# Kernel tuning notes

Measured on AMD Instinct MI355X. Metric: run time of the kernel, lower is better.

Reference implementation:

```python
import jax, jax.numpy as jnp
import numpy as np
jax.config.update("jax_enable_x64", True)  # subchunk uses float64 decays (T=128 > 24)

B, T, D = 4, 2048, 1024
H, K = 16, 64            # head_size = 64, D = H*K
CHUNK = 128              # T % 128 == 0 -> only the 128-chunk path of _chunked_wkv runs
DMIX, DDEC = 32, 64      # D_MIX_DIM, D_DECAY_DIM
PREC_MIN = 0.005
LN_EPS = 1e-5 * 8.0 ** 2 # eps * head_size_divisor**2


def setup_inputs() -> dict:
    key = jax.random.key(0)
    ks = jax.random.split(key, 24)
    f32 = jnp.float32
    rn = lambda k, s, sc=1.0: (jax.random.normal(k, s) * sc).astype(f32)
    un = lambda k, s, lo, hi: jax.random.uniform(k, s, minval=lo, maxval=hi).astype(f32)
    inv_sq = 1.0 / np.sqrt(D)
    return {
        "x": rn(ks[0], (B, T, D)),
        # token-mix interpolation coefficients (init-like: in [0,1])
        "time_maa_x": un(ks[1], (1, 1, D), 0.0, 1.0),
        "time_maa_w": un(ks[2], (1, 1, D), 0.0, 1.0),
        "time_maa_k": un(ks[3], (1, 1, D), 0.0, 1.0),
        "time_maa_v": un(ks[4], (1, 1, D), 0.0, 1.0),
        "time_maa_r": un(ks[5], (1, 1, D), 0.0, 1.0),
        "time_maa_g": un(ks[6], (1, 1, D), 0.0, 1.0),
        "time_maa_w1": rn(ks[7], (D, 5 * DMIX), 0.01),
        "time_maa_w2": un(ks[8], (5, DMIX, D), -0.01, 0.01),
        # decay: init range roughly [-6, -1] like the module
        "time_decay": un(ks[9], (1, 1, D), -6.0, -1.0),
        "time_decay_w1": rn(ks[10], (D, DDEC), 0.01),
        "time_decay_w2": un(ks[11], (DDEC, D), -0.01, 0.01),
        "time_faaaa": un(ks[12], (H, K), -0.1, 0.5),
        # projections (stored [in, out]; x @ W == nn.Linear)
        "Wr": rn(ks[13], (D, D), inv_sq),
        "Wk": rn(ks[14], (D, D), inv_sq),
        "Wv": rn(ks[15], (D, D), inv_sq),
        "Wg": rn(ks[16], (D, D), inv_sq),
        "Wo": rn(ks[17], (D, D), inv_sq),
        "ln_w": jnp.ones((D,), f32),
        "ln_b": jnp.zeros((D,), f32),
    }


def _causal_shift(x):
    # x[t-1], zero at t=0
    return jnp.pad(x[:, :-1, :], ((0, 0), (1, 0), (0, 0)))


def _chunked_wkv(r, k, v, w, u, state):
    # r,k,v,w: [B,H,L,K]; u: [1,H,1,K]; state: [B,H,K,V]
    Bb, Hh, L, Kk = r.shape
    V = v.shape[-1]
    Tc = CHUNK
    N = L // Tc
    f64 = jnp.float64

    w_decay = jnp.clip(jnp.exp(w), PREC_MIN, None)
    wc_log = jnp.log(w_decay.astype(jnp.float32)).reshape(Bb, Hh, N, Tc, Kk)
    wc_cum = jnp.cumsum(wc_log, axis=-2)                              # inclusive cumsum over chunk
    shifted = jnp.pad(wc_cum[..., :-1, :], ((0, 0),) * 3 + ((1, 0), (0, 0)))
    ws = wc_log.sum(axis=-2, keepdims=True)                           # [B,H,N,1,K] total log-decay
    w_inter = jnp.exp(ws - wc_cum).astype(r.dtype)
    w_intra = jnp.exp(wc_cum - wc_log).astype(r.dtype)

    rc = r.reshape(Bb, Hh, N, Tc, Kk)
    kc = k.reshape(Bb, Hh, N, Tc, Kk)
    vc = v.reshape(Bb, Hh, N, Tc, V)

    # intra-chunk attention in float64 with mid-chunk offset for stability
    off = shifted[..., Tc // 2:Tc // 2 + 1, :]
    r_decay = jnp.exp((shifted - off).astype(f64))
    k_inv = jnp.exp((off - wc_cum).astype(f64))
    a = jnp.einsum('bhnik,bhnjk->bhnij', rc.astype(f64) * r_decay,
                   kc.astype(f64) * k_inv).astype(r.dtype)
    a = jnp.tril(a, -1)
    diag = jnp.einsum('bhntk,bhntk->bhnt', rc, u[:, :, :, None, :] * kc)  # u bonus on the diagonal
    a = a + diag[..., None] * jnp.eye(Tc, dtype=r.dtype)
    out = jnp.einsum('bhnij,bhnjv->bhniv', a, vc)

    # inter-chunk recurrent state carry
    wkv = jnp.einsum('bhntk,bhntv->bhnkv', kc * w_inter, vc)          # per-chunk KV update
    ws_e = jnp.swapaxes(jnp.exp(ws), -1, -2).astype(r.dtype)          # [B,H,N,K,1]

    def step(s, xs):
        wkv_i, ws_i = xs
        return s * ws_i + wkv_i, s                                    # emit state BEFORE update

    state_f, states = jax.lax.scan(step, state,
                                   (jnp.moveaxis(wkv, 2, 0), jnp.moveaxis(ws_e, 2, 0)))
    states = jnp.moveaxis(states, 0, 2)                               # [B,H,N,K,V]
    out = out + jnp.einsum('bhntk,bhnkv->bhntv', rc * w_intra, states)
    return out.reshape(Bb, Hh, L, V), state_f


def reference(x, time_maa_x, time_maa_w, time_maa_k, time_maa_v, time_maa_r,
              time_maa_g, time_maa_w1, time_maa_w2, time_decay, time_decay_w1,
              time_decay_w2, time_faaaa, Wr, Wk, Wv, Wg, Wo, ln_w, ln_b):
    Bb, Tt, Dd = x.shape
    xx = _causal_shift(x) - x                                          # dxprev (recurrent mode)

    # data-dependent 5-way token-mix (RWKV-6 LoRA mix)
    xxx = jnp.tanh((x + xx * time_maa_x) @ time_maa_w1)                # [B,T,5*DMIX]
    m = jnp.einsum('btfi,fid->fbtd', xxx.reshape(Bb, Tt, 5, DMIX), time_maa_w2)
    mw, mk, mv, mr, mg = m
    xw = x + xx * (time_maa_w + mw)
    xk = x + xx * (time_maa_k + mk)
    xv = x + xx * (time_maa_v + mv)
    xr = x + xx * (time_maa_r + mr)
    xg = x + xx * (time_maa_g + mg)

    to_heads = lambda t: t.reshape(Bb, Tt, H, K).transpose(0, 2, 1, 3)  # [B,H,T,K]
    r = to_heads(xr @ Wr)
    k = to_heads(xk @ Wk)
    v = to_heads(xv @ Wv)
    g = jax.nn.silu(xg @ Wg)

    ww = time_decay + jnp.tanh(xw @ time_decay_w1) @ time_decay_w2
    w = to_heads(-jnp.exp(ww))                                         # log-decay (negative)
    u = time_faaaa.reshape(1, H, 1, K)

    state0 = jnp.zeros((Bb, H, K, K), dtype=x.dtype)
    out, _state = _chunked_wkv(r, k, v, w, u, state0)

    # GroupNorm(n_head groups) over flattened (B*T, D)
    og = out.transpose(0, 2, 1, 3).reshape(Bb * Tt, H, K)
    mu = og.mean(-1, keepdims=True)
    var = og.var(-1, keepdims=True)
    og = (og - mu) / jnp.sqrt(var + LN_EPS)
    out = (og.reshape(Bb * Tt, Dd) * ln_w + ln_b).reshape(Bb, Tt, Dd)

    return (out * g) @ Wo
```

## Files before the change

### kernel.cpp

```cpp
#include <hip/hip_runtime.h>
#include <hip/hip_bf16.h>
#include <math.h>

typedef __hip_bfloat16 bf16;
typedef __attribute__((ext_vector_type(8))) short short8;
typedef __attribute__((ext_vector_type(4))) float f32x4;

#define Tt 2048
#define Dd 1024
#define Hh 16

__device__ __forceinline__ float b2f(bf16 v){ return __bfloat162float(v); }
__device__ __forceinline__ bf16  f2b(float v){ return __float2bfloat16(v); }

__device__ __forceinline__ int seg_t(int lr, int t0, int Lm1){ return t0 + (lr & Lm1); }
__device__ __forceinline__ size_t seg_grow(int lr, int b0, int t0, int Llog2, int Lm1){
  return ((size_t)(b0 + (lr >> Llog2)) * Tt) + (size_t)seg_t(lr, t0, Lm1);
}

struct MixP { const bf16* maa[5]; bf16* dst[5]; };
struct Proj4 { const bf16* A[4]; const bf16* Bt[4]; bf16* C[4]; };

__global__ __launch_bounds__(256) void k_detect(const unsigned short* __restrict__ xs,
                                                int* __restrict__ flag){
  __shared__ int bad;
  if(threadIdx.x == 0) bad = 0;
  __syncthreads();
  int local = 0;
  for(int i = threadIdx.x; i < 8192; i += 256){
    unsigned e = (xs[i] >> 7) & 0xFF;
    if(e >= 0xC0) local++;
  }
  if(local) atomicAdd(&bad, local);
  __syncthreads();
  if(threadIdx.x == 0) flag[0] = (bad > 16) ? 1 : 0;
}

__global__ __launch_bounds__(256) void k_conv(const void* __restrict__ src,
                                              bf16* __restrict__ dst, int n,
                                              const int* __restrict__ flag){
  int i = blockIdx.x * 256 + threadIdx.x;
  if(i >= n) return;
  if(flag[0]) dst[i] = f2b(((const float*)src)[i]);
  else        dst[i] = ((const bf16*)src)[i];
}

__global__ __launch_bounds__(256) void k_transpose(const bf16* __restrict__ src,
                                                   bf16* __restrict__ dst){
  __shared__ bf16 tile[32][33];
  int bx = blockIdx.x * 32, by = blockIdx.y * 32;
  int tx = threadIdx.x & 31, ty = threadIdx.x >> 5;
  for(int r = ty; r < 32; r += 8)
    tile[r][tx] = src[(size_t)(by + r) * 1024 + bx + tx];
  __syncthreads();
  for(int r = ty; r < 32; r += 8)
    dst[(size_t)(bx + r) * 1024 + by + tx] = tile[tx][r];
}

__global__ __launch_bounds__(256) void k_transposeP(const bf16* __restrict__ src,
                                                    bf16* __restrict__ dst,
                                                    int K, int N, int Npad){
  int idx = blockIdx.x * 256 + threadIdx.x;
  if(idx >= Npad * K) return;
  int n = idx / K, k = idx - n * K;
  dst[idx] = (n < N) ? src[(size_t)k * N + n] : f2b(0.f);
}

__global__ __launch_bounds__(256) void k_prep(const bf16* __restrict__ x,
                                              const bf16* __restrict__ tmx,
                                              bf16* __restrict__ xmx,
                                              int b0, int t0, int Llog2){
  const int Lm1 = (1 << Llog2) - 1;
  int idx = blockIdx.x * 256 + threadIdx.x;
  int lr = idx >> 10, d = idx & 1023;
  size_t grow = seg_grow(lr, b0, t0, Llog2, Lm1);
  int tl = seg_t(lr, t0, Lm1);
  float xc = b2f(x[grow * Dd + d]);
  float xp = tl ? b2f(x[(grow - 1) * Dd + d]) : 0.f;
  xmx[idx] = f2b(xc + (xp - xc) * b2f(tmx[d]));
}

constexpr int GEPI_BF16 = 0, GEPI_SILU = 1, GEPI_OUT = 2;

template<int EPI>
__global__ __launch_bounds__(256) void gemm_mfma(
    const bf16* __restrict__ A,
    const bf16* __restrict__ Bt,
    void* __restrict__ Cv,
    const int* __restrict__ oflag,
    int rowoff){
  __shared__ short As[128 * 40];
  __shared__ short Bs[128 * 40];
  int tid = threadIdx.x;
  int bn = blockIdx.x * 128;
  int bm = blockIdx.y * 128;
  int w = tid >> 6, lane = tid & 63;
  int wm = (w & 1) * 64, wn = (w >> 1) * 64;
  int m16 = lane & 15, quad = lane >> 4;

  f32x4 acc[4][4];
  #pragma unroll
  for(int mi = 0; mi < 4; mi++)
    #pragma unroll
    for(int ni = 0; ni < 4; ni++)
      acc[mi][ni] = (f32x4){0.f, 0.f, 0.f, 0.f};

  int srow = tid >> 2;
  int sk8  = (tid & 3) * 8;
  const bf16* Ag = A  + (size_t)(bm + srow) * 1024 + sk8;
  const bf16* Bg = Bt + (size_t)(bn + srow) * 1024 + sk8;
  short* Aw = As + srow * 40 + sk8;
  short* Bw = Bs + srow * 40 + sk8;

  for(int kb = 0; kb < 1024; kb += 32){
    #pragma unroll
    for(int rep = 0; rep < 2; rep++){
      *(short8*)(Aw + rep * 64 * 40) = *(const short8*)(Ag + (size_t)rep * 64 * 1024 + kb);
      *(short8*)(Bw + rep * 64 * 40) = *(const short8*)(Bg + (size_t)rep * 64 * 1024 + kb);
    }
    __syncthreads();
    short8 af[4], bfr[4];
    #pragma unroll
    for(int mi = 0; mi < 4; mi++)
      af[mi] = *(const short8*)(As + (wm + mi * 16 + m16) * 40 + quad * 8);
    #pragma unroll
    for(int ni = 0; ni < 4; ni++)
      bfr[ni] = *(const short8*)(Bs + (wn + ni * 16 + m16) * 40 + quad * 8);
    #pragma unroll
    for(int mi = 0; mi < 4; mi++)
      #pragma unroll
      for(int ni = 0; ni < 4; ni++)
        acc[mi][ni] = __builtin_amdgcn_mfma_f32_16x16x32_bf16(af[mi], bfr[ni], acc[mi][ni], 0, 0, 0);
    __syncthreads();
  }
  #pragma unroll
  for(int mi = 0; mi < 4; mi++){
    #pragma unroll
    for(int ni = 0; ni < 4; ni++){
      #pragma unroll
      for(int r = 0; r < 4; r++){
        int row = bm + wm + mi * 16 + quad * 4 + r;
        int col = bn + wn + ni * 16 + m16;
        float v = acc[mi][ni][r];
        if constexpr(EPI == GEPI_BF16){
          ((bf16*)Cv)[(size_t)row * 1024 + col] = f2b(v);
        } else if constexpr(EPI == GEPI_SILU){
          ((bf16*)Cv)[(size_t)row * 1024 + col] = f2b(v / (1.f + expf(-v)));
        } else {
          size_t off = (size_t)(row + rowoff) * 1024 + col;
          if(oflag[0]) ((float*)Cv)[off] = v;
          else         ((bf16*)Cv)[off]  = f2b(v);
        }
      }
    }
  }
}

__global__ __launch_bounds__(256) void gemm_proj4(Proj4 prm){
  int z = blockIdx.z;
  const bf16* __restrict__ A  = prm.A[z];
  const bf16* __restrict__ Bt = prm.Bt[z];
  bf16* __restrict__ C        = prm.C[z];
  __shared__ short As[128 * 40];
  __shared__ short Bs[128 * 40];
  int tid = threadIdx.x;
  int bn = blockIdx.x * 128;
  int bm = blockIdx.y * 128;
  int w = tid >> 6, lane = tid & 63;
  int wm = (w & 1) * 64, wn = (w >> 1) * 64;
  int m16 = lane & 15, quad = lane >> 4;

  f32x4 acc[4][4];
  #pragma unroll
  for(int mi = 0; mi < 4; mi++)
    #pragma unroll
    for(int ni = 0; ni < 4; ni++)
      acc[mi][ni] = (f32x4){0.f, 0.f, 0.f, 0.f};

  int srow = tid >> 2;
  int sk8  = (tid & 3) * 8;
  const bf16* Ag = A  + (size_t)(bm + srow) * 1024 + sk8;
  const bf16* Bg = Bt + (size_t)(bn + srow) * 1024 + sk8;
  short* Aw = As + srow * 40 + sk8;
  short* Bw = Bs + srow * 40 + sk8;

  for(int kb = 0; kb < 1024; kb += 32){
    #pragma unroll
    for(int rep = 0; rep < 2; rep++){
      *(short8*)(Aw + rep * 64 * 40) = *(const short8*)(Ag + (size_t)rep * 64 * 1024 + kb);
      *(short8*)(Bw + rep * 64 * 40) = *(const short8*)(Bg + (size_t)rep * 64 * 1024 + kb);
    }
    __syncthreads();
    short8 af[4], bfr[4];
    #pragma unroll
    for(int mi = 0; mi < 4; mi++)
      af[mi] = *(const short8*)(As + (wm + mi * 16 + m16) * 40 + quad * 8);
    #pragma unroll
    for(int ni = 0; ni < 4; ni++)
      bfr[ni] = *(const short8*)(Bs + (wn + ni * 16 + m16) * 40 + quad * 8);
    #pragma unroll
    for(int mi = 0; mi < 4; mi++)
      #pragma unroll
      for(int ni = 0; ni < 4; ni++)
        acc[mi][ni] = __builtin_amdgcn_mfma_f32_16x16x32_bf16(af[mi], bfr[ni], acc[mi][ni], 0, 0, 0);
    __syncthreads();
  }
  bool silu = (z == 3);
  #pragma unroll
  for(int mi = 0; mi < 4; mi++){
    #pragma unroll
    for(int ni = 0; ni < 4; ni++){
      #pragma unroll
      for(int r = 0; r < 4; r++){
        int row = bm + wm + mi * 16 + quad * 4 + r;
        int col = bn + wn + ni * 16 + m16;
        float v = acc[mi][ni][r];
        if(silu) v = v / (1.f + expf(-v));
        C[(size_t)row * 1024 + col] = f2b(v);
      }
    }
  }
}

__global__ __launch_bounds__(256) void gemm_mix(
    const bf16* __restrict__ xxx,
    const bf16* __restrict__ w2T,
    const bf16* __restrict__ xg,
    MixP prm, int b0, int t0, int Llog2){
  const int Lm1 = (1 << Llog2) - 1;
  int c = blockIdx.z;
  __shared__ short As[128 * 40];
  __shared__ short Bs[128 * 40];
  int tid = threadIdx.x;
  int bn = blockIdx.x * 128;
  int bm = blockIdx.y * 128;
  int w = tid >> 6, lane = tid & 63;
  int wm = (w & 1) * 64, wn = (w >> 1) * 64;
  int m16 = lane & 15, quad = lane >> 4;

  int srow = tid >> 2;
  int sk8  = (tid & 3) * 8;
  #pragma unroll
  for(int rep = 0; rep < 2; rep++){
    *(short8*)(As + (srow + rep * 64) * 40 + sk8) =
        *(const short8*)(xxx + (size_t)(bm + srow + rep * 64) * 256 + c * 32 + sk8);
    *(short8*)(Bs + (srow + rep * 64) * 40 + sk8) =
        *(const short8*)(w2T + (size_t)c * 32768 + (size_t)(bn + srow + rep * 64) * 32 + sk8);
  }
  __syncthreads();
  f32x4 acc[4][4];
  short8 af[4], bfr[4];
  #pragma unroll
  for(int mi = 0; mi < 4; mi++)
    af[mi] = *(const short8*)(As + (wm + mi * 16 + m16) * 40 + quad * 8);
  #pragma unroll
  for(int ni = 0; ni < 4; ni++)
    bfr[ni] = *(const short8*)(Bs + (wn + ni * 16 + m16) * 40 + quad * 8);
  #pragma unroll
  for(int mi = 0; mi < 4; mi++)
    #pragma unroll
    for(int ni = 0; ni < 4; ni++)
      acc[mi][ni] = __builtin_amdgcn_mfma_f32_16x16x32_bf16(
          af[mi], bfr[ni], (f32x4){0.f, 0.f, 0.f, 0.f}, 0, 0, 0);

  const bf16* maa = prm.maa[c];
  bf16* dst = prm.dst[c];
  #pragma unroll
  for(int mi = 0; mi < 4; mi++){
    #pragma unroll
    for(int ni = 0; ni < 4; ni++){
      #pragma unroll
      for(int r = 0; r < 4; r++){
        int row = bm + wm + mi * 16 + quad * 4 + r;
        int col = bn + wn + ni * 16 + m16;
        size_t grow = seg_grow(row, b0, t0, Llog2, Lm1);
        int tl = seg_t(row, t0, Lm1);
        float xc = b2f(xg[grow * Dd + col]);
        float xp = tl ? b2f(xg[(grow - 1) * Dd + col]) : 0.f;
        dst[(size_t)row * 1024 + col] =
            f2b(xc + (xp - xc) * (b2f(maa[col]) + acc[mi][ni][r]));
      }
    }
  }
}

constexpr int G2_TANH = 0, G2_DECAY = 1;

template<int EPI>
__global__ __launch_bounds__(256) void gemm_mfma2(
    const bf16* __restrict__ A,
    const bf16* __restrict__ Bt,
    void* __restrict__ Cv, int ldc,
    int Ndim, int Kdim,
    const bf16* __restrict__ e_w){
  __shared__ short As[128 * 40];
  __shared__ short Bs[128 * 40];
  int tid = threadIdx.x;
  int bn = blockIdx.x * 128;
  int bm = blockIdx.y * 128;
  int w = tid >> 6, lane = tid & 63;
  int wm = (w & 1) * 64, wn = (w >> 1) * 64;
  int m16 = lane & 15, quad = lane >> 4;

  f32x4 acc[4][4];
  #pragma unroll
  for(int mi = 0; mi < 4; mi++)
    #pragma unroll
    for(int ni = 0; ni < 4; ni++)
      acc[mi][ni] = (f32x4){0.f, 0.f, 0.f, 0.f};

  int srow = tid >> 2;
  int sk8  = (tid & 3) * 8;
  const bf16* Ag = A  + (size_t)(bm + srow) * Kdim + sk8;
  const bf16* Bg = Bt + (size_t)(bn + srow) * Kdim + sk8;
  short* Aw = As + srow * 40 + sk8;
  short* Bw = Bs + srow * 40 + sk8;

  for(int kb = 0; kb < Kdim; kb += 32){
    #pragma unroll
    for(int rep = 0; rep < 2; rep++){
      *(short8*)(Aw + rep * 64 * 40) = *(const short8*)(Ag + (size_t)rep * 64 * Kdim + kb);
      *(short8*)(Bw + rep * 64 * 40) = *(const short8*)(Bg + (size_t)rep * 64 * Kdim + kb);
    }
    __syncthreads();
    short8 af[4], bfr[4];
    #pragma unroll
    for(int mi = 0; mi < 4; mi++)
      af[mi] = *(const short8*)(As + (wm + mi * 16 + m16) * 40 + quad * 8);
    #pragma unroll
    for(int ni = 0; ni < 4; ni++)
      bfr[ni] = *(const short8*)(Bs + (wn + ni * 16 + m16) * 40 + quad * 8);
    #pragma unroll
    for(int mi = 0; mi < 4; mi++)
      #pragma unroll
      for(int ni = 0; ni < 4; ni++)
        acc[mi][ni] = __builtin_amdgcn_mfma_f32_16x16x32_bf16(af[mi], bfr[ni], acc[mi][ni], 0, 0, 0);
    __syncthreads();
  }
  #pragma unroll
  for(int mi = 0; mi < 4; mi++){
    #pragma unroll
    for(int ni = 0; ni < 4; ni++){
      #pragma unroll
      for(int r = 0; r < 4; r++){
        int row = bm + wm + mi * 16 + quad * 4 + r;
        int col = bn + wn + ni * 16 + m16;
        if(col >= Ndim) continue;
        float v = acc[mi][ni][r];
        size_t off = (size_t)row * ldc + col;
        if constexpr(EPI == G2_TANH){
          ((bf16*)Cv)[off] = f2b(tanhf(v));
        } else {
          float td = b2f(e_w[col]) + v;
          ((float*)Cv)[off] = fmaxf(-expf(td), -5.2983173665480363f);
        }
      }
    }
  }
}

constexpr int EPI_OUTV = 5;
#define BM 64
#define BN 64
#define BK 16

template<int EPI>
__global__ __launch_bounds__(256) void gemm_ep(
    const bf16* __restrict__ A, int lda,
    const bf16* __restrict__ Bm, int ldb,
    void* __restrict__ Cv, int ldc,
    int Mdim, int Ndim, int Kdim,
    const bf16* __restrict__ xg, const bf16* __restrict__ e_w,
    int b0, int t0, int Llog2, const int* __restrict__ oflag){
  const int Lm1 = (1 << Llog2) - 1;
  __shared__ float As[BM][BK + 1];
  __shared__ float Bs[BK][BN + 4];
  int tid = threadIdx.x;
  int tx = tid & 15, ty = tid >> 4;
  int bm = blockIdx.y * BM, bn = blockIdx.x * BN;
  float acc[4][4] = {};
  for(int kb = 0; kb < Kdim; kb += BK){
    {
      int lr = tid >> 2;
      int lc = (tid & 3) * 4;
      int gr = bm + lr;
      #pragma unroll
      for(int q = 0; q < 4; q++){
        int gc = kb + lc + q;
        float av = 0.f;
        if(gr < Mdim && gc < Kdim)
          av = b2f(A[(size_t)gr * lda + gc]);
        As[lr][lc + q] = av;
      }
    }
    {
      int lr = tid >> 4;
      int lc = (tid & 15) * 4;
      #pragma unroll
      for(int q = 0; q < 4; q++){
        int gr = kb + lr; int gc = bn + lc + q;
        Bs[lr][lc + q] = (gr < Kdim && gc < Ndim) ? b2f(Bm[(size_t)gr * ldb + gc]) : 0.f;
      }
    }
    __syncthreads();
    #pragma unroll
    for(int kk = 0; kk < BK; kk++){
      float ar[4], br[4];
      #pragma unroll
      for(int q = 0; q < 4; q++) ar[q] = As[ty * 4 + q][kk];
      #pragma unroll
      for(int q = 0; q < 4; q++) br[q] = Bs[kk][tx * 4 + q];
      #pragma unroll
      for(int mi = 0; mi < 4; mi++)
        #pragma unroll
        for(int ni = 0; ni < 4; ni++)
          acc[mi][ni] += ar[mi] * br[ni];
    }
    __syncthreads();
  }
  #pragma unroll
  for(int mi = 0; mi < 4; mi++){
    int row = bm + ty * 4 + mi;
    if(row >= Mdim) continue;
    #pragma unroll
    for(int ni = 0; ni < 4; ni++){
      int col = bn + tx * 4 + ni;
      if(col >= Ndim) continue;
      float vacc = acc[mi][ni];
      size_t grow = seg_grow(row, b0, t0, Llog2, Lm1);
      size_t go = grow * Dd + col;
      if(oflag[0]) ((float*)Cv)[go] = vacc;
      else         ((bf16*)Cv)[go]  = f2b(vacc);
    }
  }
}

__global__ __launch_bounds__(256) void k_cumsum(float* __restrict__ wd,
                                                float* __restrict__ wse,
                                                int nlog2){
  int blk = blockIdx.x;
  int dg = blk & 3; int rest = blk >> 2;
  int nmask = (1 << nlog2) - 1;
  int ln = rest & nmask; int bp = rest >> nlog2;
  int d = dg * 256 + threadIdx.x;
  size_t rowbase = (((size_t)bp << nlog2) + ln) * 128;
  size_t base = rowbase * Dd + d;
  float c = 0.f;
  for(int t = 0; t < 128; t++){
    size_t ix = base + (size_t)t * Dd;
    c += wd[ix];
    wd[ix] = c;
  }
  int h = d >> 6, k0 = d & 63;
  wse[((((size_t)bp * Hh + h) << nlog2) | ln) * 64 + k0] = __expf(fminf(c, 0.f));
}

__global__ __launch_bounds__(256) void k_chunk1(const bf16* __restrict__ kb,
                                                const bf16* __restrict__ vb,
                                                const float* __restrict__ wcum,
                                                float* __restrict__ wkv,
                                                int nlog2){
  __shared__ __align__(16) bf16 ktT[64 * 136];
  __shared__ __align__(16) bf16 vT2[64 * 136];
  int tid = threadIdx.x, blk = blockIdx.x;
  int nmask = (1 << nlog2) - 1;
  int ln = blk & nmask; int rest = blk >> nlog2;
  int h = rest & 15; int bp = rest >> 4;
  size_t rowbase = (((size_t)bp << nlog2) + ln) * 128;
  size_t gbase = rowbase * Dd + h * 64;
  for(int r = 0; r < 32; r++){
    int idx = r * 256 + tid;
    int t0 = idx >> 6, k0 = idx & 63;
    size_t gi = gbase + (size_t)t0 * Dd + k0;
    float c  = wcum[gi];
    float cL = wcum[gbase + (size_t)127 * Dd + k0];
    ktT[k0 * 136 + t0] = f2b(b2f(kb[gi]) * __expf(fminf(cL - c, 0.f)));
    vT2[k0 * 136 + t0] = vb[gi];
  }
  __syncthreads();
  int w = tid >> 6, lane = tid & 63;
  int m16 = lane & 15, quad = lane >> 4;
  f32x4 acc[4];
  #pragma unroll
  for(int nt = 0; nt < 4; nt++) acc[nt] = (f32x4){0.f, 0.f, 0.f, 0.f};
  #pragma unroll
  for(int ks = 0; ks < 4; ks++){
    short8 af = *(const short8*)(ktT + (w * 16 + m16) * 136 + ks * 32 + quad * 8);
    #pragma unroll
    for(int nt = 0; nt < 4; nt++){
      short8 bfr = *(const short8*)(vT2 + (nt * 16 + m16) * 136 + ks * 32 + quad * 8);
      acc[nt] = __builtin_amdgcn_mfma_f32_16x16x32_bf16(af, bfr, acc[nt], 0, 0, 0);
    }
  }
  size_t obase = (size_t)blk * 4096;
  #pragma unroll
  for(int nt = 0; nt < 4; nt++)
    #pragma unroll
    for(int r = 0; r < 4; r++)
      wkv[obase + (size_t)(w * 16 + quad * 4 + r) * 64 + nt * 16 + m16] = acc[nt][r];
}

__global__ __launch_bounds__(256) void k_scan(float* __restrict__ buf,
                                              const float* __restrict__ wse,
                                              float* __restrict__ st,
                                              int b0, int firstseg, int nlog2){
  int blk = blockIdx.x;
  int h = blk & 15, bp = blk >> 4;
  int tid = threadIdx.x;
  size_t stbase = ((size_t)(b0 + bp) * Hh + h) * 4096;
  int nloc = 1 << nlog2;
  float s[16];
  #pragma unroll
  for(int r = 0; r < 16; r++)
    s[r] = firstseg ? 0.f : st[stbase + r * 256 + tid];
  for(int ln = 0; ln < nloc; ln++){
    size_t idx = (((size_t)bp * Hh + h) << nlog2) | ln;
    size_t base = idx * 4096;
    const float* wsp = wse + idx * 64;
    #pragma unroll
    for(int r = 0; r < 16; r++){
      int e = r * 256 + tid;
      float tmp = buf[base + e];
      buf[base + e] = s[r];
      s[r] = s[r] * wsp[e >> 6] + tmp;
    }
  }
  #pragma unroll
  for(int r = 0; r < 16; r++)
    st[stbase + r * 256 + tid] = s[r];
}

__global__ __launch_bounds__(256) void k_chunk2(
    const bf16* __restrict__ rb, const bf16* __restrict__ kb,
    const bf16* __restrict__ vb, const float* __restrict__ wcum,
    const float* __restrict__ states, const bf16* __restrict__ u,
    float* __restrict__ outw, int nlog2){
  __shared__ __align__(16) bf16 vT[64 * 136];
  __shared__ __align__(16) bf16 sT[64 * 72];
  __shared__ __align__(16) bf16 ascr[4 * 16 * 136];
  int tid = threadIdx.x, blk = blockIdx.x;
  int nmask = (1 << nlog2) - 1;
  int ln = blk & nmask; int rest = blk >> nlog2;
  int h = rest & 15; int bp = rest >> 4;
  size_t rowbase = (((size_t)bp << nlog2) + ln) * 128;
  size_t gbase = rowbase * Dd + h * 64;
  for(int r = 0; r < 32; r++){
    int idx = r * 256 + tid;
    int t0 = idx >> 6, v0 = idx & 63;
    vT[v0 * 136 + t0] = vb[gbase + (size_t)t0 * Dd + v0];
  }
  for(int r = 0; r < 16; r++){
    int idx = r * 256 + tid;
    int k0 = idx >> 6, v0 = idx & 63;
    sT[v0 * 72 + k0] = f2b(states[(size_t)blk * 4096 + k0 * 64 + v0]);
  }
  __syncthreads();
  int w = tid >> 6, lane = tid & 63;
  int m16 = lane & 15, quad = lane >> 4;
  bf16* scr = ascr + w * (16 * 136);
  f32x4 oacc[2][4];
  #pragma unroll
  for(int a1 = 0; a1 < 2; a1++)
    #pragma unroll
    for(int a2 = 0; a2 < 4; a2++) oacc[a1][a2] = (f32x4){0.f, 0.f, 0.f, 0.f};

  for(int ii = 0; ii < 2; ii++){
    int I = ii ? (7 - w) : w;
    int B = I * 16;
    for(int z = lane; z < 544; z += 64) ((unsigned long long*)scr)[z] = 0ULL;
    int i0 = B + m16;
    size_t rowi = rowbase + i0;
    short8 rf[2], af[2], rw2[2];
    float crv[2][8];
    #pragma unroll
    for(int ks = 0; ks < 2; ks++){
      int koff = h * 64 + ks * 32 + quad * 8;
      rf[ks] = *(const short8*)(rb + rowi * Dd + koff);
      float cp[8];
      if(i0 > 0){
        f32x4 c0 = *(const f32x4*)(wcum + (rowi - 1) * Dd + koff);
        f32x4 c1 = *(const f32x4*)(wcum + (rowi - 1) * Dd + koff + 4);
        #pragma unroll
        for(int c = 0; c < 4; c++){ cp[c] = c0[c]; cp[4 + c] = c1[c]; }
      } else {
        #pragma unroll
        for(int c = 0; c < 8; c++) cp[c] = 0.f;
      }
      if(B > 0){
        f32x4 c0 = *(const f32x4*)(wcum + (rowbase + B - 1) * Dd + koff);
        f32x4 c1 = *(const f32x4*)(wcum + (rowbase + B - 1) * Dd + koff + 4);
        #pragma unroll
        for(int c = 0; c < 4; c++){ crv[ks][c] = c0[c]; crv[ks][4 + c] = c1[c]; }
      } else {
        #pragma unroll
        for(int c = 0; c < 8; c++) crv[ks][c] = 0.f;
      }
      short8 av, wv;
      #pragma unroll
      for(int c = 0; c < 8; c++){
        float rv = b2f(((const bf16*)&rf[ks])[c]);
        ((bf16*)&av)[c] = f2b(rv * __expf(fminf(cp[c] - crv[ks][c], 0.f)));
        ((bf16*)&wv)[c] = f2b(rv * __expf(fminf(cp[c], 0.f)));
      }
      af[ks] = av; rw2[ks] = wv;
    }
    for(int J = 0; J < I; J++){
      f32x4 aacc = (f32x4){0.f, 0.f, 0.f, 0.f};
      #pragma unroll
      for(int ks = 0; ks < 2; ks++){
        int koff = h * 64 + ks * 32 + quad * 8;
        size_t rowj = rowbase + J * 16 + m16;
        short8 k8 = *(const short8*)(kb + rowj * Dd + koff);
        f32x4 c0 = *(const f32x4*)(wcum + rowj * Dd + koff);
        f32x4 c1 = *(const f32x4*)(wcum + rowj * Dd + koff + 4);
        short8 bfrag;
        #pragma unroll
        for(int c = 0; c < 8; c++){
          float kv = b2f(((const bf16*)&k8)[c]);
          float cj = (c < 4) ? c0[c] : c1[c - 4];
          ((bf16*)&bfrag)[c] = f2b(kv * __expf(fminf(crv[ks][c] - cj, 0.f)));
        }
        aacc = __builtin_amdgcn_mfma_f32_16x16x32_bf16(af[ks], bfrag, aacc, 0, 0, 0);
      }
      #pragma unroll
      for(int r = 0; r < 4; r++)
        scr[(quad * 4 + r) * 136 + J * 16 + m16] = f2b(aacc[r]);
    }
    {
      f32x4 aacc = (f32x4){0.f, 0.f, 0.f, 0.f};
      f32x4 dacc = (f32x4){0.f, 0.f, 0.f, 0.f};
      #pragma unroll
      for(int ks = 0; ks < 2; ks++){
        int koff = h * 64 + ks * 32 + quad * 8;
        size_t rowj = rowbase + B + m16;
        short8 k8 = *(const short8*)(kb + rowj * Dd + koff);
        f32x4 c0 = *(const f32x4*)(wcum + rowj * Dd + koff);
        f32x4 c1 = *(const f32x4*)(wcum + rowj * Dd + koff + 4);
        short8 u8 = *(const short8*)(u + h * 64 + ks * 32 + quad * 8);
        short8 bf1, bf2;
        #pragma unroll
        for(int c = 0; c < 8; c++){
          float kv = b2f(((const bf16*)&k8)[c]);
          float cj = (c < 4) ? c0[c] : c1[c - 4];
          ((bf16*)&bf1)[c] = f2b(kv * __expf(crv[ks][c] - cj));
          ((bf16*)&bf2)[c] = f2b(kv * b2f(((const bf16*)&u8)[c]));
        }
        aacc = __builtin_amdgcn_mfma_f32_16x16x32_bf16(af[ks], bf1, aacc, 0, 0, 0);
        dacc = __builtin_amdgcn_mfma_f32_16x16x32_bf16(rf[ks], bf2, dacc, 0, 0, 0);
      }
      #pragma unroll
      for(int r = 0; r < 4; r++){
        int row = quad * 4 + r, col = m16;
        if(col < row)       scr[row * 136 + B + col] = f2b(aacc[r]);
        else if(col == row) scr[row * 136 + B + col] = f2b(dacc[r]);
      }
    }
    asm volatile("s_waitcnt lgkmcnt(0)" ::: "memory");
    int nks = (I + 2) >> 1;
    for(int ks2 = 0; ks2 < nks; ks2++){
      short8 afr = *(const short8*)(scr + m16 * 136 + ks2 * 32 + quad * 8);
      #pragma unroll
      for(int nt = 0; nt < 4; nt++){
        short8 bfr = *(const short8*)(vT + (nt * 16 + m16) * 136 + ks2 * 32 + quad * 8);
        oacc[ii][nt] = __builtin_amdgcn_mfma_f32_16x16x32_bf16(afr, bfr, oacc[ii][nt], 0, 0, 0);
      }
    }
    #pragma unroll
    for(int ks = 0; ks < 2; ks++){
      #pragma unroll
      for(int nt = 0; nt < 4; nt++){
        short8 sfr = *(const short8*)(sT + (nt * 16 + m16) * 72 + ks * 32 + quad * 8);
        oacc[ii][nt] = __builtin_amdgcn_mfma_f32_16x16x32_bf16(rw2[ks], sfr, oacc[ii][nt], 0, 0, 0);
      }
    }
  }
  __syncthreads();
  #pragma unroll
  for(int ii = 0; ii < 2; ii++){
    int I = ii ? (7 - w) : w;
    int B = I * 16;
    #pragma unroll
    for(int nt = 0; nt < 4; nt++){
      #pragma unroll
      for(int r = 0; r < 4; r++){
        int i0 = B + quad * 4 + r;
        int v0 = nt * 16 + m16;
        outw[gbase + (size_t)i0 * Dd + v0] = oacc[ii][nt][r];
      }
    }
  }
}

__global__ __launch_bounds__(256) void k_norm(const float* __restrict__ outw,
                                              const bf16* __restrict__ gb,
                                              const bf16* __restrict__ lnw,
                                              const bf16* __restrict__ lnb,
                                              bf16* __restrict__ gated){
  int lr = blockIdx.x;
  int wv = threadIdx.x >> 6, lane = threadIdx.x & 63;
  for(int hh = wv; hh < Hh; hh += 4){
    size_t ix = (size_t)lr * Dd + hh * 64 + lane;
    float xv = outw[ix];
    float s1 = xv, s2 = xv * xv;
    #pragma unroll
    for(int off = 32; off > 0; off >>= 1){
      s1 += __shfl_xor(s1, off);
      s2 += __shfl_xor(s2, off);
    }
    float mu  = s1 * 0.015625f;
    float var = s2 * 0.015625f - mu * mu;
    float inv = rsqrtf(var + 6.4e-4f);
    float og  = (xv - mu) * inv * b2f(lnw[hh * 64 + lane]) + b2f(lnb[hh * 64 + lane]);
    gated[ix] = f2b(og * b2f(gb[ix]));
  }
}

extern "C" void kernel_launch(void* const* d_in, const int* in_sizes, int n_in,
                              void* d_out, int out_size, void* d_ws, size_t ws_size,
                              hipStream_t stream){
  char* W = (char*)d_ws;
  size_t cur = 0;
  auto carve = [&](size_t bytes) -> char* {
    char* p = W + cur;
    cur = (cur + bytes + 255) & ~(size_t)255;
    return p;
  };

  int* flag = (int*)carve(4096);
  static const int NEL[20] = {8388608, 1024, 1024, 1024, 1024, 1024, 1024,
                              163840, 163840, 1024, 65536, 65536, 1024,
                              1048576, 1048576, 1048576, 1048576, 1048576,
                              1024, 1024};
  bf16* canon[20];
  for(int i = 0; i < 20; i++) canon[i] = (bf16*)carve((size_t)NEL[i] * 2);

  k_detect<<<dim3(1), 256, 0, stream>>>((const unsigned short*)d_in[0], flag);
  for(int i = 0; i < 20; i++)
    k_conv<<<dim3((NEL[i] + 255) / 256), 256, 0, stream>>>(d_in[i], canon[i], NEL[i], flag);

  const bf16* xp   = canon[0];
  const bf16* tmx  = canon[1];
  const bf16* tdec = canon[9];
  const bf16* up   = canon[12];
  const bf16* lnwp = canon[18];
  const bf16* lnbp = canon[19];

  bf16* WrT  = (bf16*)carve(2097152);
  bf16* WkT  = (bf16*)carve(2097152);
  bf16* WvT  = (bf16*)carve(2097152);
  bf16* WgT  = (bf16*)carve(2097152);
  bf16* WoT  = (bf16*)carve(2097152);
  bf16* W1T  = (bf16*)carve(256 * 1024 * 2);
  bf16* DW1T = (bf16*)carve(128 * 1024 * 2);
  bf16* DW2T = (bf16*)carve(1024 * 64 * 2);
  bf16* W2T  = (bf16*)carve(5 * 1024 * 32 * 2);
  k_transpose<<<dim3(32, 32), 256, 0, stream>>>(canon[13], WrT);
  k_transpose<<<dim3(32, 32), 256, 0, stream>>>(canon[14], WkT);
  k_transpose<<<dim3(32, 32), 256, 0, stream>>>(canon[15], WvT);
  k_transpose<<<dim3(32, 32), 256, 0, stream>>>(canon[16], WgT);
  k_transpose<<<dim3(32, 32), 256, 0, stream>>>(canon[17], WoT);
  k_transposeP<<<dim3(1024), 256, 0, stream>>>(canon[7],  W1T,  1024, 160, 256);
  k_transposeP<<<dim3(512),  256, 0, stream>>>(canon[10], DW1T, 1024, 64, 128);
  k_transposeP<<<dim3(256),  256, 0, stream>>>(canon[11], DW2T, 64, 1024, 1024);
  for(int c = 0; c < 5; c++)
    k_transposeP<<<dim3(128), 256, 0, stream>>>(canon[8] + (size_t)c * 32768,
                                                W2T + (size_t)c * 32768, 32, 1024, 1024);

  float* st = (float*)carve(1u << 20);
  size_t FIXED = cur;

  const size_t UNIT = 19104, PAD = 65536;
  int nb, L;
  if(ws_size >= FIXED + (size_t)8192 * UNIT + PAD){ nb = 4; L = 2048; }
  else {
    nb = 1; L = 2048;
    while(L > 128 && ws_size < FIXED + (size_t)L * UNIT + PAD) L >>= 1;
  }
  const int Llog2 = __builtin_ctz((unsigned)L);
  const int nlog2 = Llog2 - 7;
  const int M     = nb * L;
  const size_t Mr = (size_t)M;

  bf16*  xxx    = (bf16*) carve(Mr * 512);
  bf16*  ww1    = (bf16*) carve(Mr * 128);
  float* wse    = (float*)carve(Mr * 32);
  bf16*  xmx    = (bf16*) carve(Mr * 2048);
  bf16*  mixbuf = (bf16*) carve(Mr * 2048);
  bf16*  kbuf   = (bf16*) carve(Mr * 2048);
  bf16*  vbuf   = (bf16*) carve(Mr * 2048);
  bf16*  rbuf   = (bf16*) carve(Mr * 2048);
  bf16*  gbuf   = (bf16*) carve(Mr * 2048);
  float* wdec   = (float*)carve(Mr * 4096);
  float* wkvst  = (float*)carve(Mr * 2048);
  float* outw   = wdec;
  bf16*  gated  = mixbuf;

  MixP mp;
  mp.maa[0] = canon[2]; mp.maa[1] = canon[3]; mp.maa[2] = canon[4];
  mp.maa[3] = canon[5]; mp.maa[4] = canon[6];
  mp.dst[0] = mixbuf;
  mp.dst[1] = (bf16*)wdec;
  mp.dst[2] = (bf16*)wdec + Mr * 1024;
  mp.dst[3] = (bf16*)wkvst;
  mp.dst[4] = xmx;

  Proj4 pp;
  pp.A[0] = mp.dst[1]; pp.Bt[0] = WkT; pp.C[0] = kbuf;
  pp.A[1] = mp.dst[2]; pp.Bt[1] = WvT; pp.C[1] = vbuf;
  pp.A[2] = mp.dst[3]; pp.Bt[2] = WrT; pp.C[2] = rbuf;
  pp.A[3] = mp.dst[4]; pp.Bt[3] = WgT; pp.C[3] = gbuf;

  for(int b0 = 0; b0 < 4; b0 += nb){
    for(int t0 = 0; t0 < Tt; t0 += L){
      k_prep<<<dim3(M * 4), 256, 0, stream>>>(xp, tmx, xmx, b0, t0, Llog2);
      gemm_mfma2<G2_TANH><<<dim3(2, M/128), 256, 0, stream>>>(
          xmx, W1T, xxx, 256, 160, 1024, nullptr);
      gemm_mix<<<dim3(8, M/128, 5), 256, 0, stream>>>(
          xxx, W2T, xp, mp, b0, t0, Llog2);
      gemm_proj4<<<dim3(8, M/128, 4), 256, 0, stream>>>(pp);
      gemm_mfma2<G2_TANH><<<dim3(1, M/128), 256, 0, stream>>>(
          mixbuf, DW1T, ww1, 64, 64, 1024, nullptr);
      gemm_mfma2<G2_DECAY><<<dim3(8, M/128), 256, 0, stream>>>(
          ww1, DW2T, wdec, 1024, 1024, 64, tdec);
      int nloc = 1 << nlog2;
      k_cumsum<<<dim3(nb * nloc * 4), 256, 0, stream>>>(wdec, wse, nlog2);
      k_chunk1<<<dim3(nb * 16 * nloc), 256, 0, stream>>>(kbuf, vbuf, wdec, wkvst, nlog2);
      k_scan<<<dim3(nb * 16), 256, 0, stream>>>(wkvst, wse, st, b0, (t0 == 0) ? 1 : 0, nlog2);
      k_chunk2<<<dim3(nb * 16 * nloc), 256, 0, stream>>>(rbuf, kbuf, vbuf, wdec, wkvst, up, outw, nlog2);
      k_norm<<<dim3(M), 256, 0, stream>>>(outw, gbuf, lnwp, lnbp, gated);
      if(L == Tt){
        gemm_mfma<GEPI_OUT><<<dim3(8, M/128), 256, 0, stream>>>(gated, WoT, d_out, flag, b0 * Tt);
      } else {
        gemm_ep<EPI_OUTV><<<dim3(16, M/64), 256, 0, stream>>>(
            gated, 1024, canon[17], 1024, d_out, 1024, M, 1024, 1024,
            nullptr, nullptr, b0, t0, Llog2, flag);
      }
    }
  }
}
```

Baseline: 635.0 us.

## Use direct global-to-LDS async loads in GEMMs and batch setup kernel launches

All MFMA GEMM kernels now fill their shared-memory tiles with global_load_lds instead of staging through registers. The padded 40-short row stride becomes an unpadded 32-short layout, which the per-wave contiguous LDS writes of global_load_lds require. Separately, the 20 per-input conversion launches are merged into one vectorized kernel, and the five weight transposes and five W2 transposes are each merged into a single batched launch. The goal is less register traffic in the GEMM load path and less launch overhead, at the risk of more LDS bank conflicts on the fragment reads now that the padding is gone.

```diff
diff --git a/kernel.cpp b/kernel.cpp
--- a/kernel.cpp
+++ b/kernel.cpp
@@ -1,9 +1,11 @@
 #include <hip/hip_runtime.h>
 #include <hip/hip_bf16.h>
 #include <math.h>
+#include <stdint.h>
 
 typedef __hip_bfloat16 bf16;
 typedef __attribute__((ext_vector_type(8))) short short8;
+typedef __attribute__((ext_vector_type(4))) short short4v;
 typedef __attribute__((ext_vector_type(4))) float f32x4;
 
 #define Tt 2048
@@ -13,6 +15,13 @@
 __device__ __forceinline__ float b2f(bf16 v){ return __bfloat162float(v); }
 __device__ __forceinline__ bf16  f2b(float v){ return __float2bfloat16(v); }
 
+__device__ __forceinline__ void async16(const void* g, void* l){
+  __builtin_amdgcn_global_load_lds(
+      (__attribute__((address_space(1))) void*)(g),
+      (__attribute__((address_space(3))) void*)(l),
+      16, 0, 0);
+}
+
 __device__ __forceinline__ int seg_t(int lr, int t0, int Lm1){ return t0 + (lr & Lm1); }
 __device__ __forceinline__ size_t seg_grow(int lr, int b0, int t0, int Llog2, int Lm1){
   return ((size_t)(b0 + (lr >> Llog2)) * Tt) + (size_t)seg_t(lr, t0, Lm1);
@@ -20,6 +29,8 @@
 
 struct MixP { const bf16* maa[5]; bf16* dst[5]; };
 struct Proj4 { const bf16* A[4]; const bf16* Bt[4]; bf16* C[4]; };
+struct ConvP { const void* src[20]; bf16* dst[20]; };
+struct T5P  { const bf16* src[5]; bf16* dst[5]; };
 
 __global__ __launch_bounds__(256) void k_detect(const unsigned short* __restrict__ xs,
                                                 int* __restrict__ flag){
@@ -36,18 +47,32 @@
   if(threadIdx.x == 0) flag[0] = (bad > 16) ? 1 : 0;
 }
 
-__global__ __launch_bounds__(256) void k_conv(const void* __restrict__ src,
-                                              bf16* __restrict__ dst, int n,
-                                              const int* __restrict__ flag){
-  int i = blockIdx.x * 256 + threadIdx.x;
-  if(i >= n) return;
-  if(flag[0]) dst[i] = f2b(((const float*)src)[i]);
-  else        dst[i] = ((const bf16*)src)[i];
-}
-
-__global__ __launch_bounds__(256) void k_transpose(const bf16* __restrict__ src,
-                                                   bf16* __restrict__ dst){
+__global__ __launch_bounds__(256) void k_conv_all(ConvP p, const int* __restrict__ flag){
+  const int PRE[21] = {0,8388608,8389632,8390656,8391680,8392704,8393728,8394752,
+                       8558592,8722432,8723456,8788992,8854528,8855552,9904128,
+                       10952704,12001280,13049856,14098432,14099456,14100480};
+  int v = (blockIdx.x * 256 + threadIdx.x) * 4;
+  if(v >= 14100480) return;
+  int a = 0;
+  #pragma unroll
+  for(int i = 1; i < 20; i++) if(v >= PRE[i]) a = i;
+  int off = v - PRE[a];
+  bf16* d = p.dst[a] + off;
+  if(flag[0]){
+    f32x4 xv = *(const f32x4*)((const float*)p.src[a] + off);
+    short4v o;
+    #pragma unroll
+    for(int j = 0; j < 4; j++) ((bf16*)&o)[j] = f2b(xv[j]);
+    *(short4v*)d = o;
+  } else {
+    *(short4v*)d = *(const short4v*)((const short*)p.src[a] + off);
+  }
+}
+
+__global__ __launch_bounds__(256) void k_transpose5(T5P p){
   __shared__ bf16 tile[32][33];
+  const bf16* __restrict__ src = p.src[blockIdx.z];
+  bf16* __restrict__ dst       = p.dst[blockIdx.z];
   int bx = blockIdx.x * 32, by = blockIdx.y * 32;
   int tx = threadIdx.x & 31, ty = threadIdx.x >> 5;
   for(int r = ty; r < 32; r += 8)
@@ -64,6 +89,14 @@
   if(idx >= Npad * K) return;
   int n = idx / K, k = idx - n * K;
   dst[idx] = (n < N) ? src[(size_t)k * N + n] : f2b(0.f);
+}
+
+__global__ __launch_bounds__(256) void k_transposeP5(const bf16* __restrict__ src,
+                                                     bf16* __restrict__ dst){
+  int z = blockIdx.z;
+  int idx = blockIdx.x * 256 + threadIdx.x;
+  int n = idx >> 5, k = idx & 31;
+  dst[(size_t)z * 32768 + idx] = src[(size_t)z * 32768 + (size_t)k * 1024 + n];
 }
 
 __global__ __launch_bounds__(256) void k_prep(const bf16* __restrict__ x,
@@ -89,8 +122,8 @@
     void* __restrict__ Cv,
     const int* __restrict__ oflag,
     int rowoff){
-  __shared__ short As[128 * 40];
-  __shared__ short Bs[128 * 40];
+  __shared__ __align__(16) short As[128 * 32];
+  __shared__ __align__(16) short Bs[128 * 32];
   int tid = threadIdx.x;
   int bn = blockIdx.x * 128;
   int bm = blockIdx.y * 128;
@@ -109,23 +142,23 @@
   int sk8  = (tid & 3) * 8;
   const bf16* Ag = A  + (size_t)(bm + srow) * 1024 + sk8;
   const bf16* Bg = Bt + (size_t)(bn + srow) * 1024 + sk8;
-  short* Aw = As + srow * 40 + sk8;
-  short* Bw = Bs + srow * 40 + sk8;
+  short* Al = As + w * 512;
+  short* Bl = Bs + w * 512;
 
   for(int kb = 0; kb < 1024; kb += 32){
     #pragma unroll
     for(int rep = 0; rep < 2; rep++){
-      *(short8*)(Aw + rep * 64 * 40) = *(const short8*)(Ag + (size_t)rep * 64 * 1024 + kb);
-      *(short8*)(Bw + rep * 64 * 40) = *(const short8*)(Bg + (size_t)rep * 64 * 1024 + kb);
+      async16(Ag + (size_t)rep * 64 * 1024 + kb, Al + rep * 2048);
+      async16(Bg + (size_t)rep * 64 * 1024 + kb, Bl + rep * 2048);
     }
     __syncthreads();
     short8 af[4], bfr[4];
     #pragma unroll
     for(int mi = 0; mi < 4; mi++)
-      af[mi] = *(const short8*)(As + (wm + mi * 16 + m16) * 40 + quad * 8);
+      af[mi] = *(const short8*)(As + (wm + mi * 16 + m16) * 32 + quad * 8);
     #pragma unroll
     for(int ni = 0; ni < 4; ni++)
-      bfr[ni] = *(const short8*)(Bs + (wn + ni * 16 + m16) * 40 + quad * 8);
+      bfr[ni] = *(const short8*)(Bs + (wn + ni * 16 + m16) * 32 + quad * 8);
     #pragma unroll
     for(int mi = 0; mi < 4; mi++)
       #pragma unroll
@@ -161,8 +194,8 @@
   const bf16* __restrict__ A  = prm.A[z];
   const bf16* __restrict__ Bt = prm.Bt[z];
   bf16* __restrict__ C        = prm.C[z];
-  __shared__ short As[128 * 40];
-  __shared__ short Bs[128 * 40];
+  __shared__ __align__(16) short As[128 * 32];
+  __shared__ __align__(16) short Bs[128 * 32];
   int tid = threadIdx.x;
   int bn = blockIdx.x * 128;
   int bm = blockIdx.y * 128;
@@ -181,23 +214,23 @@
   int sk8  = (tid & 3) * 8;
   const bf16* Ag = A  + (size_t)(bm + srow) * 1024 + sk8;
   const bf16* Bg = Bt + (size_t)(bn + srow) * 1024 + sk8;
-  short* Aw = As + srow * 40 + sk8;
-  short* Bw = Bs + srow * 40 + sk8;
+  short* Al = As + w * 512;
+  short* Bl = Bs + w * 512;
 
   for(int kb = 0; kb < 1024; kb += 32){
     #pragma unroll
     for(int rep = 0; rep < 2; rep++){
-      *(short8*)(Aw + rep * 64 * 40) = *(const short8*)(Ag + (size_t)rep * 64 * 1024 + kb);
-      *(short8*)(Bw + rep * 64 * 40) = *(const short8*)(Bg + (size_t)rep * 64 * 1024 + kb);
+      async16(Ag + (size_t)rep * 64 * 1024 + kb, Al + rep * 2048);
+      async16(Bg + (size_t)rep * 64 * 1024 + kb, Bl + rep * 2048);
     }
     __syncthreads();
     short8 af[4], bfr[4];
     #pragma unroll
     for(int mi = 0; mi < 4; mi++)
-      af[mi] = *(const short8*)(As + (wm + mi * 16 + m16) * 40 + quad * 8);
+      af[mi] = *(const short8*)(As + (wm + mi * 16 + m16) * 32 + quad * 8);
     #pragma unroll
     for(int ni = 0; ni < 4; ni++)
-      bfr[ni] = *(const short8*)(Bs + (wn + ni * 16 + m16) * 40 + quad * 8);
+      bfr[ni] = *(const short8*)(Bs + (wn + ni * 16 + m16) * 32 + quad * 8);
     #pragma unroll
     for(int mi = 0; mi < 4; mi++)
       #pragma unroll
@@ -229,8 +262,8 @@
     MixP prm, int b0, int t0, int Llog2){
   const int Lm1 = (1 << Llog2) - 1;
   int c = blockIdx.z;
-  __shared__ short As[128 * 40];
-  __shared__ short Bs[128 * 40];
+  __shared__ __align__(16) short As[128 * 32];
+  __shared__ __align__(16) short Bs[128 * 32];
   int tid = threadIdx.x;
   int bn = blockIdx.x * 128;
   int bm = blockIdx.y * 128;
@@ -240,22 +273,22 @@
 
   int srow = tid >> 2;
   int sk8  = (tid & 3) * 8;
+  short* Al = As + w * 512;
+  short* Bl = Bs + w * 512;
   #pragma unroll
   for(int rep = 0; rep < 2; rep++){
-    *(short8*)(As + (srow + rep * 64) * 40 + sk8) =
-        *(const short8*)(xxx + (size_t)(bm + srow + rep * 64) * 256 + c * 32 + sk8);
-    *(short8*)(Bs + (srow + rep * 64) * 40 + sk8) =
-        *(const short8*)(w2T + (size_t)c * 32768 + (size_t)(bn + srow + rep * 64) * 32 + sk8);
+    async16(xxx + (size_t)(bm + srow + rep * 64) * 256 + c * 32 + sk8, Al + rep * 2048);
+    async16(w2T + (size_t)c * 32768 + (size_t)(bn + srow + rep * 64) * 32 + sk8, Bl + rep * 2048);
   }
   __syncthreads();
   f32x4 acc[4][4];
   short8 af[4], bfr[4];
   #pragma unroll
   for(int mi = 0; mi < 4; mi++)
-    af[mi] = *(const short8*)(As + (wm + mi * 16 + m16) * 40 + quad * 8);
+    af[mi] = *(const short8*)(As + (wm + mi * 16 + m16) * 32 + quad * 8);
   #pragma unroll
   for(int ni = 0; ni < 4; ni++)
-    bfr[ni] = *(const short8*)(Bs + (wn + ni * 16 + m16) * 40 + quad * 8);
+    bfr[ni] = *(const short8*)(Bs + (wn + ni * 16 + m16) * 32 + quad * 8);
   #pragma unroll
   for(int mi = 0; mi < 4; mi++)
     #pragma unroll
@@ -293,8 +326,8 @@
     void* __restrict__ Cv, int ldc,
     int Ndim, int Kdim,
     const bf16* __restrict__ e_w){
-  __shared__ short As[128 * 40];
-  __shared__ short Bs[128 * 40];
+  __shared__ __align__(16) short As[128 * 32];
+  __shared__ __align__(16) short Bs[128 * 32];
   int tid = threadIdx.x;
   int bn = blockIdx.x * 128;
   int bm = blockIdx.y * 128;
@@ -313,23 +346,23 @@
   int sk8  = (tid & 3) * 8;
   const bf16* Ag = A  + (size_t)(bm + srow) * Kdim + sk8;
   const bf16* Bg = Bt + (size_t)(bn + srow) * Kdim + sk8;
-  short* Aw = As + srow * 40 + sk8;
-  short* Bw = Bs + srow * 40 + sk8;
+  short* Al = As + w * 512;
+  short* Bl = Bs + w * 512;
 
   for(int kb = 0; kb < Kdim; kb += 32){
     #pragma unroll
     for(int rep = 0; rep < 2; rep++){
-      *(short8*)(Aw + rep * 64 * 40) = *(const short8*)(Ag + (size_t)rep * 64 * Kdim + kb);
-      *(short8*)(Bw + rep * 64 * 40) = *(const short8*)(Bg + (size_t)rep * 64 * Kdim + kb);
+      async16(Ag + (size_t)rep * 64 * Kdim + kb, Al + rep * 2048);
+      async16(Bg + (size_t)rep * 64 * Kdim + kb, Bl + rep * 2048);
     }
     __syncthreads();
     short8 af[4], bfr[4];
     #pragma unroll
     for(int mi = 0; mi < 4; mi++)
-      af[mi] = *(const short8*)(As + (wm + mi * 16 + m16) * 40 + quad * 8);
+      af[mi] = *(const short8*)(As + (wm + mi * 16 + m16) * 32 + quad * 8);
     #pragma unroll
     for(int ni = 0; ni < 4; ni++)
-      bfr[ni] = *(const short8*)(Bs + (wn + ni * 16 + m16) * 40 + quad * 8);
+      bfr[ni] = *(const short8*)(Bs + (wn + ni * 16 + m16) * 32 + quad * 8);
     #pragma unroll
     for(int mi = 0; mi < 4; mi++)
       #pragma unroll
@@ -735,8 +768,9 @@
   for(int i = 0; i < 20; i++) canon[i] = (bf16*)carve((size_t)NEL[i] * 2);
 
   k_detect<<<dim3(1), 256, 0, stream>>>((const unsigned short*)d_in[0], flag);
-  for(int i = 0; i < 20; i++)
-    k_conv<<<dim3((NEL[i] + 255) / 256), 256, 0, stream>>>(d_in[i], canon[i], NEL[i], flag);
+  ConvP cp;
+  for(int i = 0; i < 20; i++){ cp.src[i] = d_in[i]; cp.dst[i] = canon[i]; }
+  k_conv_all<<<dim3(13770), 256, 0, stream>>>(cp, flag);
 
   const bf16* xp   = canon[0];
   const bf16* tmx  = canon[1];
@@ -754,17 +788,17 @@
   bf16* DW1T = (bf16*)carve(128 * 1024 * 2);
   bf16* DW2T = (bf16*)carve(1024 * 64 * 2);
   bf16* W2T  = (bf16*)carve(5 * 1024 * 32 * 2);
-  k_transpose<<<dim3(32, 32), 256, 0, stream>>>(canon[13], WrT);
-  k_transpose<<<dim3(32, 32), 256, 0, stream>>>(canon[14], WkT);
-  k_transpose<<<dim3(32, 32), 256, 0, stream>>>(canon[15], WvT);
-  k_transpose<<<dim3(32, 32), 256, 0, stream>>>(canon[16], WgT);
-  k_transpose<<<dim3(32, 32), 256, 0, stream>>>(canon[17], WoT);
+  T5P tp;
+  tp.src[0] = canon[13]; tp.dst[0] = WrT;
+  tp.src[1] = canon[14]; tp.dst[1] = WkT;
+  tp.src[2] = canon[15]; tp.dst[2] = WvT;
+  tp.src[3] = canon[16]; tp.dst[3] = WgT;
+  tp.src[4] = canon[17]; tp.dst[4] = WoT;
+  k_transpose5<<<dim3(32, 32, 5), 256, 0, stream>>>(tp);
   k_transposeP<<<dim3(1024), 256, 0, stream>>>(canon[7],  W1T,  1024, 160, 256);
   k_transposeP<<<dim3(512),  256, 0, stream>>>(canon[10], DW1T, 1024, 64, 128);
   k_transposeP<<<dim3(256),  256, 0, stream>>>(canon[11], DW2T, 64, 1024, 1024);
-  for(int c = 0; c < 5; c++)
-    k_transposeP<<<dim3(128), 256, 0, stream>>>(canon[8] + (size_t)c * 32768,
-                                                W2T + (size_t)c * 32768, 32, 1024, 1024);
+  k_transposeP5<<<dim3(128, 1, 5), 256, 0, stream>>>(canon[8], W2T);
 
   float* st = (float*)carve(1u << 20);
   size_t FIXED = cur;
```

Measured after the change: 569.1 us. 1.12x faster.
